# Kernel tuning notes

Hardware: AMD Instinct MI355X
Metric: run time of the kernel (lower is better)

## Reference

```python
import jax, jax.numpy as jnp
import numpy as np

B, N, E, D, R, T, L = 4, 20000, 320000, 64, 64, 1000, 6
LN_EPS = 1e-5


def setup_inputs() -> dict:
    key = jax.random.key(0)
    ks = jax.random.split(key, 20)
    inp = {
        "edge_index": jax.random.randint(ks[0], (2, E), 0, N),
        "edge_type": jax.random.randint(ks[1], (E,), 0, R),
        "relation_representations": jax.random.normal(ks[2], (B, R, D), jnp.float32),
        "h_index": jax.random.randint(ks[3], (B,), 0, N),
        "r_index": jax.random.randint(ks[4], (B,), 0, R),
        "t_index": jax.random.randint(ks[5], (B, T), 0, N),
        "edge_weight": jnp.ones((E,), jnp.float32),
        # per-layer relation-projection MLP (Linear,ReLU,Linear)
        "rp_w1": jax.random.normal(ks[6], (L, D, D), jnp.float32) / np.sqrt(D),
        "rp_b1": jnp.zeros((L, D), jnp.float32),
        "rp_w2": jax.random.normal(ks[7], (L, D, D), jnp.float32) / np.sqrt(D),
        "rp_b2": jnp.zeros((L, D), jnp.float32),
        # per-layer update linear: concat([input, aggregated]) -> D
        "conv_w": jax.random.normal(ks[8], (L, 2 * D, D), jnp.float32) / np.sqrt(2 * D),
        "conv_b": jnp.zeros((L, D), jnp.float32),
        "ln_g": jnp.ones((L, D), jnp.float32),
        "ln_b": jnp.zeros((L, D), jnp.float32),
        # final MLP (num_mlp_layers=2): feature_dim = D (last hidden) + D (query) = 2D
        "mlp_w1": jax.random.normal(ks[9], (2 * D, 2 * D), jnp.float32) / np.sqrt(2 * D),
        "mlp_b1": jnp.zeros((2 * D,), jnp.float32),
        "mlp_w2": jax.random.normal(ks[10], (2 * D, 1), jnp.float32) / np.sqrt(2 * D),
        "mlp_b2": jnp.zeros((1,), jnp.float32),
    }
    return inp


def reference(edge_index, edge_type, relation_representations, h_index, r_index,
              t_index, edge_weight, rp_w1, rp_b1, rp_w2, rp_b2, conv_w, conv_b,
              ln_g, ln_b, mlp_w1, mlp_b1, mlp_w2, mlp_b2):
    # --- boundary: scatter query embedding onto source node per query ---
    query = relation_representations[jnp.arange(B), r_index]              # [B, D]
    boundary = jnp.zeros((B, N, D), jnp.float32).at[jnp.arange(B), h_index].add(query)
    src, dst = edge_index[0], edge_index[1]

    def layer(x, params):
        w1, b1, w2, b2, cw, cb, g, b = params
        # project_relations MLP on query relation representations
        rel = jax.nn.relu(jnp.einsum('brd,de->bre', relation_representations, w1) + b1)
        rel = jnp.einsum('brd,de->bre', rel, w2) + b2                     # [B, R, D]
        # distmult message: h[src] * rel[edge_type], weighted
        msg = x[:, src, :] * rel[:, edge_type, :] * edge_weight[None, :, None]  # [B, E, D]
        agg = jax.ops.segment_sum(msg.transpose(1, 0, 2), dst,
                                  num_segments=N).transpose(1, 0, 2)
        agg = agg + boundary                                              # boundary self-loop
        h = jnp.concatenate([x, agg], axis=-1) @ cw + cb                  # [B, N, D]
        mu = h.mean(-1, keepdims=True)
        var = h.var(-1, keepdims=True)
        h = (h - mu) * jax.lax.rsqrt(var + LN_EPS) * g + b                # layer norm
        h = jax.nn.relu(h)
        return h + x, None                                                # short_cut

    x, _ = jax.lax.scan(layer, boundary,
                        (rp_w1, rp_b1, rp_w2, rp_b2, conv_w, conv_b, ln_g, ln_b))
    node_query = jnp.broadcast_to(query[:, None, :], (B, N, D))
    output = jnp.concatenate([x, node_query], axis=-1)                    # [B, N, 2D]
    feat = jnp.take_along_axis(output, t_index[:, :, None], axis=1)       # [B, T, 2D]
    h = jax.nn.relu(feat @ mlp_w1 + mlp_b1)
    score = (h @ mlp_w2 + mlp_b2).squeeze(-1)                             # [B, T]
    return score
```

## Files before the change

### kernel.cpp

```cpp
#include <hip/hip_runtime.h>
#include <hip/hip_fp16.h>

#define NB 4
#define NN 20000
#define NE 320000
#define ND 64
#define NR 64
#define NT 1000
#define NL 6
#define LN_EPS 1e-5f
#define CAP 64

typedef _Float16 half8 __attribute__((ext_vector_type(8)));
typedef _Float16 half4v __attribute__((ext_vector_type(4)));
typedef float floatx4 __attribute__((ext_vector_type(4)));


__global__ void __launch_bounds__(256)
prep1(int* __restrict__ cnt,
      const float* __restrict__ cw, _Float16* __restrict__ cwt,
      const float* __restrict__ relrep, const int* __restrict__ r_index,
      float* __restrict__ query,
      const float* __restrict__ rp_w1, const float* __restrict__ rp_b1,
      const float* __restrict__ rp_w2, const float* __restrict__ rp_b2,
      __half* __restrict__ rel16) {
    int blk = blockIdx.x, tid = threadIdx.x;
    if (blk < 79) {
        int i = blk * 256 + tid;
        if (i < NN) cnt[i] = 0;
    } else if (blk < 271) {
        int i = (blk - 79) * 256 + tid;
        int l = i >> 13, rem = i & 8191, k = rem >> 6, n = rem & 63;
        cwt[l * 8192 + n * 128 + k] = (_Float16)cw[i];
    } else if (blk == 271) {
        int b = tid >> 6, d = tid & 63;
        query[tid] = relrep[(b * NR + r_index[b]) * ND + d];
    } else {
        int u = blk - 272;
        int l = u >> 6, r = u & 63;
        int b = tid >> 6, j = tid & 63;
        const float* w1 = rp_w1 + l * ND * ND;
        const float* w2 = rp_w2 + l * ND * ND;
        float xin = relrep[(b * NR + r) * ND + j];
        float acc = rp_b1[l * ND + j];
        #pragma unroll 8
        for (int k = 0; k < ND; ++k) acc += __shfl(xin, k) * w1[k * ND + j];
        float hmid = fmaxf(acc, 0.f);
        float outv = rp_b2[l * ND + j];
        #pragma unroll 8
        for (int k = 0; k < ND; ++k) outv += __shfl(hmid, k) * w2[k * ND + j];
        rel16[l * (NR * NB * ND) + (r * NB + b) * ND + j] = __float2half(outv);
    }
}

__global__ void __launch_bounds__(256)
prep2(const int* __restrict__ ei, const int* __restrict__ et,
      const float* __restrict__ ew, int* __restrict__ cnt,
      int4* __restrict__ epack) {
    int e = blockIdx.x * 256 + threadIdx.x;
    int d = ei[NE + e];
    int p = atomicAdd(&cnt[d], 1);
    if (p < CAP)
        epack[d * CAP + p] = make_int4(ei[e], et[e], __float_as_int(ew[e]), 0);
}

__device__ __forceinline__ float2 h2f(unsigned u) {
    __half2 h = *(__half2*)&u;
    return __half22float2(h);
}
__device__ __forceinline__ __half2 u2h2(unsigned u) { return *(__half2*)&u; }

__device__ __forceinline__ void conv_ln_epilogue(
        _Float16* A16, float* sD, int wv, int lane, int n,
        const _Float16* __restrict__ cwt, const float* __restrict__ cb,
        const float* __restrict__ g, const float* __restrict__ bb,
        __half* __restrict__ xo16) {
    __syncthreads();
    {
        int m = lane & 15, quad = lane >> 4;
        int ncol = wv * 16 + m;
        floatx4 acc = {0.f, 0.f, 0.f, 0.f};
        #pragma unroll
        for (int k0 = 0; k0 < 128; k0 += 32) {
            half8 a = *(const half8*)&A16[m * 136 + k0 + quad * 8];
            half8 bfr = *(const half8*)&cwt[ncol * 128 + k0 + quad * 8];
            acc = __builtin_amdgcn_mfma_f32_16x16x32_f16(a, bfr, acc, 0, 0, 0);
        }
        #pragma unroll
        for (int rg = 0; rg < 4; ++rg)
            sD[(quad * 4 + rg) * 65 + ncol] = acc[rg];
    }
    __syncthreads();
    float gl = g[lane], bl = bb[lane], cbl = cb[lane];
    #pragma unroll
    for (int b = 0; b < NB; ++b) {
        float acc = sD[(wv * 4 + b) * 65 + lane] + cbl;
        float s = acc, s2 = acc * acc;
        #pragma unroll
        for (int o = 32; o > 0; o >>= 1) { s += __shfl_xor(s, o); s2 += __shfl_xor(s2, o); }
        float mu  = s * (1.f / ND);
        float var = s2 * (1.f / ND) - mu * mu;
        float hn  = (acc - mu) * rsqrtf(var + LN_EPS) * gl + bl;
        float xvf = (float)A16[(wv * 4 + b) * 136 + lane];
        float v   = fmaxf(hn, 0.f) + xvf;
        xo16[(n * NB + b) * ND + lane] = __float2half(v);
    }
}

__global__ void __launch_bounds__(256)
fused_layer_first(const __half* __restrict__ rel16,
                  const int* __restrict__ cnt, const int4* __restrict__ epack,
                  const float* __restrict__ query, const int* __restrict__ h_index,
                  const _Float16* __restrict__ cwt, const float* __restrict__ cb,
                  const float* __restrict__ g, const float* __restrict__ bb,
                  __half* __restrict__ xo16) {
    __shared__ _Float16 A16[16 * 136];
    __shared__ float sD[16 * 65];
    int wv = threadIdx.x >> 6;
    int lane = threadIdx.x & 63;
    int n = blockIdx.x * 4 + wv;
    int cn = min(cnt[n], CAP);
    int bidx = lane >> 4, c4 = (lane & 15) << 2;
    int hb = h_index[bidx];

    const uint2* __restrict__ r2 = (const uint2*)rel16;
    float4 q4 = ((const float4*)query)[lane];
    half4v qh;
    qh.x = (_Float16)q4.x; qh.y = (_Float16)q4.y;
    qh.z = (_Float16)q4.z; qh.w = (_Float16)q4.w;
    float qx = (float)qh.x, qy = (float)qh.y, qz = (float)qh.z, qw = (float)qh.w;

    float4 agg4 = make_float4(0.f, 0.f, 0.f, 0.f);
    {
        int4 ed = make_int4(0, 0, 0, 0);
        if (lane < cn) ed = epack[n * CAP + lane];
        for (int j = 0; j < cn; ++j) {
            int s   = __shfl(ed.x, j);
            int t   = __shfl(ed.y, j);
            float w = __int_as_float(__shfl(ed.z, j));
            if (s == hb) {
                uint2 ra = r2[t * 64 + lane];
                float2 q0 = h2f(ra.x), q1 = h2f(ra.y);
                agg4.x = fmaf(qx * q0.x, w, agg4.x);
                agg4.y = fmaf(qy * q0.y, w, agg4.y);
                agg4.z = fmaf(qz * q1.x, w, agg4.z);
                agg4.w = fmaf(qw * q1.y, w, agg4.w);
            }
        }
    }
    if (n == hb) {
        agg4.x += q4.x; agg4.y += q4.y; agg4.z += q4.z; agg4.w += q4.w;
    }
    {
        int r = wv * 4 + bidx;
        half4v xh = {0, 0, 0, 0};
        if (n == hb) xh = qh;
        *(half4v*)&A16[r * 136 + c4] = xh;
        half4v ah;
        ah.x = (_Float16)agg4.x; ah.y = (_Float16)agg4.y;
        ah.z = (_Float16)agg4.z; ah.w = (_Float16)agg4.w;
        *(half4v*)&A16[r * 136 + 64 + c4] = ah;
    }
    conv_ln_epilogue(A16, sD, wv, lane, n, cwt, cb, g, bb, xo16);
}

#define ACCUM(xv, rv, wv_) do {                                   \
    __half2 p0 = __hmul2(u2h2((xv).x), u2h2((rv).x));             \
    __half2 p1 = __hmul2(u2h2((xv).y), u2h2((rv).y));             \
    __half2 p2 = __hmul2(u2h2((xv).z), u2h2((rv).z));             \
    __half2 p3 = __hmul2(u2h2((xv).w), u2h2((rv).w));             \
    acc[0] = fmaf(__low2float(p0),  (wv_), acc[0]);               \
    acc[1] = fmaf(__high2float(p0), (wv_), acc[1]);               \
    acc[2] = fmaf(__low2float(p1),  (wv_), acc[2]);               \
    acc[3] = fmaf(__high2float(p1), (wv_), acc[3]);               \
    acc[4] = fmaf(__low2float(p2),  (wv_), acc[4]);               \
    acc[5] = fmaf(__high2float(p2), (wv_), acc[5]);               \
    acc[6] = fmaf(__low2float(p3),  (wv_), acc[6]);               \
    acc[7] = fmaf(__high2float(p3), (wv_), acc[7]);               \
} while (0)

__global__ void __launch_bounds__(256, 4)
fused_layer(const __half* __restrict__ x16, const __half* __restrict__ rel16,
            const int* __restrict__ cnt, const int4* __restrict__ epack,
            const float* __restrict__ query, const int* __restrict__ h_index,
            const _Float16* __restrict__ cwt, const float* __restrict__ cb,
            const float* __restrict__ g, const float* __restrict__ bb,
            __half* __restrict__ xo16) {
    __shared__ _Float16 A16[16 * 136];
    __shared__ float sD[16 * 65];
    int wv = threadIdx.x >> 6;
    int lane = threadIdx.x & 63;
    int n = blockIdx.x * 4 + wv;
    int cn = min(cnt[n], CAP);
    int hf = lane >> 5, sub = lane & 31;

    const uint4* __restrict__ x4 = (const uint4*)x16;
    const uint4* __restrict__ r4 = (const uint4*)rel16;

    const uint2* __restrict__ x2 = (const uint2*)x16;
    uint2 xraw = x2[(n * NB + (lane >> 4)) * 16 + (lane & 15)];

    float acc[8] = {0.f, 0.f, 0.f, 0.f, 0.f, 0.f, 0.f, 0.f};
    {
        int4 ed = make_int4(0, 0, 0, 0);
        if (lane < cn) ed = epack[n * CAP + lane];
        int cmax = (cn + 3) & ~3;
        if (cmax) {
            int ja = hf, jb = 2 + hf;
            int sa = __shfl(ed.x, ja), ta = __shfl(ed.y, ja);
            int sb = __shfl(ed.x, jb), tb = __shfl(ed.y, jb);
            float wa = __int_as_float(__shfl(ed.z, ja));
            float wb = __int_as_float(__shfl(ed.z, jb));
            uint4 xa = x4[sa * 32 + sub], ra = r4[ta * 32 + sub];
            uint4 xb = x4[sb * 32 + sub], rb = r4[tb * 32 + sub];
            for (int j = 4; j < cmax; j += 4) {
                int jc = j + hf, jd = j + 2 + hf;
                int sc = __shfl(ed.x, jc), tc = __shfl(ed.y, jc);
                int sd = __shfl(ed.x, jd), td = __shfl(ed.y, jd);
                float wc = __int_as_float(__shfl(ed.z, jc));
                float wd = __int_as_float(__shfl(ed.z, jd));
                uint4 xc = x4[sc * 32 + sub], rc = r4[tc * 32 + sub];
                uint4 xd = x4[sd * 32 + sub], rd = r4[td * 32 + sub];
                ACCUM(xa, ra, wa);
                ACCUM(xb, rb, wb);
                xa = xc; ra = rc; wa = wc;
                xb = xd; rb = rd; wb = wd;
            }
            ACCUM(xa, ra, wa);
            ACCUM(xb, rb, wb);
        }
    }
    #pragma unroll
    for (int k = 0; k < 8; ++k) acc[k] += __shfl_xor(acc[k], 32);
    int bq = sub >> 3, ch = (sub & 7) << 3;
    if (hf == 0) {
        if (n == h_index[bq]) {
            const float* qp = query + bq * 64 + ch;
            #pragma unroll
            for (int k = 0; k < 8; ++k) acc[k] += qp[k];
        }
        int r = wv * 4 + bq;
        half8 ah;
        #pragma unroll
        for (int k = 0; k < 8; ++k) ah[k] = (_Float16)acc[k];
        *(half8*)&A16[r * 136 + 64 + ch] = ah;
    }
    {
        int bidx = lane >> 4, c4 = (lane & 15) << 2;
        int r = wv * 4 + bidx;
        *(uint2*)&A16[r * 136 + c4] = xraw;
    }
    conv_ln_epilogue(A16, sD, wv, lane, n, cwt, cb, g, bb, xo16);
}

__global__ void final_score(const __half* __restrict__ x16, const float* __restrict__ query,
                            const int* __restrict__ t_index,
                            const float* __restrict__ w1, const float* __restrict__ b1,
                            const float* __restrict__ w2, const float* __restrict__ b2,
                            float* __restrict__ out) {
    int gid = blockIdx.x * 4 + (threadIdx.x >> 6);
    int lane = threadIdx.x & 63;
    int b = gid / NT;
    int ti = t_index[gid];
    float xv = __half2float(x16[(ti * NB + b) * ND + lane]);
    float qv = query[b * ND + lane];
    float a0 = b1[lane], a1 = b1[lane + 64];
    #pragma unroll 8
    for (int k = 0; k < ND; ++k) {
        float f = __shfl(xv, k);
        a0 += f * w1[k * 128 + lane];
        a1 += f * w1[k * 128 + lane + 64];
    }
    #pragma unroll 8
    for (int k = 0; k < ND; ++k) {
        float f = __shfl(qv, k);
        a0 += f * w1[(ND + k) * 128 + lane];
        a1 += f * w1[(ND + k) * 128 + lane + 64];
    }
    a0 = fmaxf(a0, 0.f);
    a1 = fmaxf(a1, 0.f);
    float p = a0 * w2[lane] + a1 * w2[lane + 64];
    #pragma unroll
    for (int o = 32; o > 0; o >>= 1) p += __shfl_xor(p, o);
    if (lane == 0) out[gid] = p + b2[0];
}

extern "C" void kernel_launch(void* const* d_in, const int* in_sizes, int n_in,
                              void* d_out, int out_size, void* d_ws, size_t ws_size,
                              hipStream_t stream) {
    const int*   edge_index  = (const int*)d_in[0];
    const int*   edge_type   = (const int*)d_in[1];
    const float* relrep      = (const float*)d_in[2];
    const int*   h_index     = (const int*)d_in[3];
    const int*   r_index     = (const int*)d_in[4];
    const int*   t_index     = (const int*)d_in[5];
    const float* edge_weight = (const float*)d_in[6];
    const float* rp_w1  = (const float*)d_in[7];
    const float* rp_b1  = (const float*)d_in[8];
    const float* rp_w2  = (const float*)d_in[9];
    const float* rp_b2  = (const float*)d_in[10];
    const float* conv_w = (const float*)d_in[11];
    const float* conv_b = (const float*)d_in[12];
    const float* ln_g   = (const float*)d_in[13];
    const float* ln_b   = (const float*)d_in[14];
    const float* mlp_w1 = (const float*)d_in[15];
    const float* mlp_b1 = (const float*)d_in[16];
    const float* mlp_w2 = (const float*)d_in[17];
    const float* mlp_b2 = (const float*)d_in[18];
    float* out = (float*)d_out;

    const int BND = NB * NN * ND;
    const int RELSZ = NR * NB * ND;
    float*    ws     = (float*)d_ws;
    float*    query  = ws;
    __half*   rel16  = (__half*)(query + 256);
    __half*   x16a   = rel16 + NL * RELSZ;
    __half*   x16b   = x16a + BND;
    _Float16* cwt16  = (_Float16*)(x16b + BND);
    int4*     epack  = (int4*)(cwt16 + NL * 8192);
    int*      cnt    = (int*)(epack + NN * CAP);

    prep1<<<656, 256, 0, stream>>>(cnt, conv_w, cwt16, relrep, r_index, query,
                                   rp_w1, rp_b1, rp_w2, rp_b2, rel16);
    prep2<<<NE / 256, 256, 0, stream>>>(edge_index, edge_type, edge_weight,
                                        cnt, epack);

    __half* mc = x16a; __half* mn = x16b;
    fused_layer_first<<<NN / 4, 256, 0, stream>>>(rel16, cnt, epack,
                                                  query, h_index,
                                                  cwt16, conv_b, ln_g, ln_b, mc);
    for (int l = 1; l < NL; ++l) {
        fused_layer<<<NN / 4, 256, 0, stream>>>(mc, rel16 + l * RELSZ, cnt, epack,
                                                query, h_index,
                                                cwt16 + l * 8192, conv_b + l * ND,
                                                ln_g + l * ND, ln_b + l * ND, mn);
        __half* th = mc; mc = mn; mn = th;
    }
    final_score<<<NB * NT / 4, 256, 0, stream>>>(mc, query, t_index,
                                                 mlp_w1, mlp_b1, mlp_w2, mlp_b2, out);
}
```

Before: 329.9 us.

## Sort nodes by in-degree so each block processes similar-degree nodes

```diff
diff --git a/kernel.cpp b/kernel.cpp
--- a/kernel.cpp
+++ b/kernel.cpp
@@ -20,7 +20,7 @@
 prep1(int* __restrict__ cnt,
       const float* __restrict__ cw, _Float16* __restrict__ cwt,
       const float* __restrict__ relrep, const int* __restrict__ r_index,
-      float* __restrict__ query,
+      float* __restrict__ query, int* __restrict__ hist,
       const float* __restrict__ rp_w1, const float* __restrict__ rp_b1,
       const float* __restrict__ rp_w2, const float* __restrict__ rp_b2,
       __half* __restrict__ rel16) {
@@ -35,6 +35,7 @@
     } else if (blk == 271) {
         int b = tid >> 6, d = tid & 63;
         query[tid] = relrep[(b * NR + r_index[b]) * ND + d];
+        if (tid < 96) hist[tid] = 0;
     } else {
         int u = blk - 272;
         int l = u >> 6, r = u & 63;
@@ -64,6 +65,29 @@
         epack[d * CAP + p] = make_int4(ei[e], et[e], __float_as_int(ew[e]), 0);
 }
 
+__global__ void __launch_bounds__(256)
+prep3a(const int* __restrict__ cnt, int* __restrict__ hist) {
+    int n = blockIdx.x * 256 + threadIdx.x;
+    if (n < NN) atomicAdd(&hist[min(cnt[n], CAP)], 1);
+}
+
+__global__ void prep3b(const int* __restrict__ hist, int* __restrict__ off) {
+    if (threadIdx.x == 0) {
+        int acc = 0;
+        for (int c = CAP; c >= 0; --c) { off[c] = acc; acc += hist[c]; }
+    }
+}
+
+__global__ void __launch_bounds__(256)
+prep3c(const int* __restrict__ cnt, int* __restrict__ off,
+       int* __restrict__ perm) {
+    int n = blockIdx.x * 256 + threadIdx.x;
+    if (n < NN) {
+        int p = atomicAdd(&off[min(cnt[n], CAP)], 1);
+        perm[p] = n;
+    }
+}
+
 __device__ __forceinline__ float2 h2f(unsigned u) {
     __half2 h = *(__half2*)&u;
     return __half22float2(h);
@@ -110,6 +134,7 @@
 __global__ void __launch_bounds__(256)
 fused_layer_first(const __half* __restrict__ rel16,
                   const int* __restrict__ cnt, const int4* __restrict__ epack,
+                  const int* __restrict__ perm,
                   const float* __restrict__ query, const int* __restrict__ h_index,
                   const _Float16* __restrict__ cwt, const float* __restrict__ cb,
                   const float* __restrict__ g, const float* __restrict__ bb,
@@ -118,7 +143,7 @@
     __shared__ float sD[16 * 65];
     int wv = threadIdx.x >> 6;
     int lane = threadIdx.x & 63;
-    int n = blockIdx.x * 4 + wv;
+    int n = perm[blockIdx.x * 4 + wv];
     int cn = min(cnt[n], CAP);
     int bidx = lane >> 4, c4 = (lane & 15) << 2;
     int hb = h_index[bidx];
@@ -182,6 +207,7 @@
 __global__ void __launch_bounds__(256, 4)
 fused_layer(const __half* __restrict__ x16, const __half* __restrict__ rel16,
             const int* __restrict__ cnt, const int4* __restrict__ epack,
+            const int* __restrict__ perm,
             const float* __restrict__ query, const int* __restrict__ h_index,
             const _Float16* __restrict__ cwt, const float* __restrict__ cb,
             const float* __restrict__ g, const float* __restrict__ bb,
@@ -190,7 +216,7 @@
     __shared__ float sD[16 * 65];
     int wv = threadIdx.x >> 6;
     int lane = threadIdx.x & 63;
-    int n = blockIdx.x * 4 + wv;
+    int n = perm[blockIdx.x * 4 + wv];
     int cn = min(cnt[n], CAP);
     int hf = lane >> 5, sub = lane & 31;
 
@@ -319,19 +345,25 @@
     _Float16* cwt16  = (_Float16*)(x16b + BND);
     int4*     epack  = (int4*)(cwt16 + NL * 8192);
     int*      cnt    = (int*)(epack + NN * CAP);
+    int*      perm   = cnt + NN;
+    int*      hist   = perm + NN;
+    int*      off    = hist + 96;
 
     prep1<<<656, 256, 0, stream>>>(cnt, conv_w, cwt16, relrep, r_index, query,
-                                   rp_w1, rp_b1, rp_w2, rp_b2, rel16);
+                                   hist, rp_w1, rp_b1, rp_w2, rp_b2, rel16);
     prep2<<<NE / 256, 256, 0, stream>>>(edge_index, edge_type, edge_weight,
                                         cnt, epack);
+    prep3a<<<79, 256, 0, stream>>>(cnt, hist);
+    prep3b<<<1, 64, 0, stream>>>(hist, off);
+    prep3c<<<79, 256, 0, stream>>>(cnt, off, perm);
 
     __half* mc = x16a; __half* mn = x16b;
-    fused_layer_first<<<NN / 4, 256, 0, stream>>>(rel16, cnt, epack,
+    fused_layer_first<<<NN / 4, 256, 0, stream>>>(rel16, cnt, epack, perm,
                                                   query, h_index,
                                                   cwt16, conv_b, ln_g, ln_b, mc);
     for (int l = 1; l < NL; ++l) {
         fused_layer<<<NN / 4, 256, 0, stream>>>(mc, rel16 + l * RELSZ, cnt, epack,
-                                                query, h_index,
+                                                perm, query, h_index,
                                                 cwt16 + l * 8192, conv_b + l * ND,
                                                 ln_g + l * ND, ln_b + l * ND, mn);
         __half* th = mc; mc = mn; mn = th;
```

Measured after the change: 438.8 us. 33.0% more time.

## Gather one edge per wave with uint2 loads and scalar readlane broadcasts

Applied to the files above, without the earlier changes.

```diff
diff --git a/kernel.cpp b/kernel.cpp
--- a/kernel.cpp
+++ b/kernel.cpp
@@ -119,7 +119,7 @@
     int wv = threadIdx.x >> 6;
     int lane = threadIdx.x & 63;
     int n = blockIdx.x * 4 + wv;
-    int cn = min(cnt[n], CAP);
+    int cn = __builtin_amdgcn_readfirstlane(min(cnt[n], CAP));
     int bidx = lane >> 4, c4 = (lane & 15) << 2;
     int hb = h_index[bidx];
 
@@ -135,9 +135,9 @@
         int4 ed = make_int4(0, 0, 0, 0);
         if (lane < cn) ed = epack[n * CAP + lane];
         for (int j = 0; j < cn; ++j) {
-            int s   = __shfl(ed.x, j);
-            int t   = __shfl(ed.y, j);
-            float w = __int_as_float(__shfl(ed.z, j));
+            int s   = __builtin_amdgcn_readlane(ed.x, j);
+            int t   = __builtin_amdgcn_readlane(ed.y, j);
+            float w = __int_as_float(__builtin_amdgcn_readlane(ed.z, j));
             if (s == hb) {
                 uint2 ra = r2[t * 64 + lane];
                 float2 q0 = h2f(ra.x), q1 = h2f(ra.y);
@@ -164,22 +164,7 @@
     conv_ln_epilogue(A16, sD, wv, lane, n, cwt, cb, g, bb, xo16);
 }
 
-#define ACCUM(xv, rv, wv_) do {                                   \
-    __half2 p0 = __hmul2(u2h2((xv).x), u2h2((rv).x));             \
-    __half2 p1 = __hmul2(u2h2((xv).y), u2h2((rv).y));             \
-    __half2 p2 = __hmul2(u2h2((xv).z), u2h2((rv).z));             \
-    __half2 p3 = __hmul2(u2h2((xv).w), u2h2((rv).w));             \
-    acc[0] = fmaf(__low2float(p0),  (wv_), acc[0]);               \
-    acc[1] = fmaf(__high2float(p0), (wv_), acc[1]);               \
-    acc[2] = fmaf(__low2float(p1),  (wv_), acc[2]);               \
-    acc[3] = fmaf(__high2float(p1), (wv_), acc[3]);               \
-    acc[4] = fmaf(__low2float(p2),  (wv_), acc[4]);               \
-    acc[5] = fmaf(__high2float(p2), (wv_), acc[5]);               \
-    acc[6] = fmaf(__low2float(p3),  (wv_), acc[6]);               \
-    acc[7] = fmaf(__high2float(p3), (wv_), acc[7]);               \
-} while (0)
-
-__global__ void __launch_bounds__(256, 4)
+__global__ void __launch_bounds__(256)
 fused_layer(const __half* __restrict__ x16, const __half* __restrict__ rel16,
             const int* __restrict__ cnt, const int4* __restrict__ epack,
             const float* __restrict__ query, const int* __restrict__ h_index,
@@ -191,63 +176,43 @@
     int wv = threadIdx.x >> 6;
     int lane = threadIdx.x & 63;
     int n = blockIdx.x * 4 + wv;
-    int cn = min(cnt[n], CAP);
-    int hf = lane >> 5, sub = lane & 31;
-
-    const uint4* __restrict__ x4 = (const uint4*)x16;
-    const uint4* __restrict__ r4 = (const uint4*)rel16;
+    int cn = __builtin_amdgcn_readfirstlane(min(cnt[n], CAP));
+    int bidx = lane >> 4, c4 = (lane & 15) << 2;
+    int hb = h_index[bidx];
 
     const uint2* __restrict__ x2 = (const uint2*)x16;
-    uint2 xraw = x2[(n * NB + (lane >> 4)) * 16 + (lane & 15)];
-
-    float acc[8] = {0.f, 0.f, 0.f, 0.f, 0.f, 0.f, 0.f, 0.f};
+    const uint2* __restrict__ r2 = (const uint2*)rel16;
+
+    uint2 xraw = x2[n * 64 + lane];
+
+    float4 acc = make_float4(0.f, 0.f, 0.f, 0.f);
     {
         int4 ed = make_int4(0, 0, 0, 0);
         if (lane < cn) ed = epack[n * CAP + lane];
-        int cmax = (cn + 3) & ~3;
-        if (cmax) {
-            int ja = hf, jb = 2 + hf;
-            int sa = __shfl(ed.x, ja), ta = __shfl(ed.y, ja);
-            int sb = __shfl(ed.x, jb), tb = __shfl(ed.y, jb);
-            float wa = __int_as_float(__shfl(ed.z, ja));
-            float wb = __int_as_float(__shfl(ed.z, jb));
-            uint4 xa = x4[sa * 32 + sub], ra = r4[ta * 32 + sub];
-            uint4 xb = x4[sb * 32 + sub], rb = r4[tb * 32 + sub];
-            for (int j = 4; j < cmax; j += 4) {
-                int jc = j + hf, jd = j + 2 + hf;
-                int sc = __shfl(ed.x, jc), tc = __shfl(ed.y, jc);
-                int sd = __shfl(ed.x, jd), td = __shfl(ed.y, jd);
-                float wc = __int_as_float(__shfl(ed.z, jc));
-                float wd = __int_as_float(__shfl(ed.z, jd));
-                uint4 xc = x4[sc * 32 + sub], rc = r4[tc * 32 + sub];
-                uint4 xd = x4[sd * 32 + sub], rd = r4[td * 32 + sub];
-                ACCUM(xa, ra, wa);
-                ACCUM(xb, rb, wb);
-                xa = xc; ra = rc; wa = wc;
-                xb = xd; rb = rd; wb = wd;
-            }
-            ACCUM(xa, ra, wa);
-            ACCUM(xb, rb, wb);
+        for (int j = 0; j < cn; ++j) {
+            int s   = __builtin_amdgcn_readlane(ed.x, j);
+            int t   = __builtin_amdgcn_readlane(ed.y, j);
+            float w = __int_as_float(__builtin_amdgcn_readlane(ed.z, j));
+            uint2 xa = x2[s * 64 + lane];
+            uint2 ra = r2[t * 64 + lane];
+            __half2 p0 = __hmul2(u2h2(xa.x), u2h2(ra.x));
+            __half2 p1 = __hmul2(u2h2(xa.y), u2h2(ra.y));
+            acc.x = fmaf(__low2float(p0),  w, acc.x);
+            acc.y = fmaf(__high2float(p0), w, acc.y);
+            acc.z = fmaf(__low2float(p1),  w, acc.z);
+            acc.w = fmaf(__high2float(p1), w, acc.w);
         }
     }
-    #pragma unroll
-    for (int k = 0; k < 8; ++k) acc[k] += __shfl_xor(acc[k], 32);
-    int bq = sub >> 3, ch = (sub & 7) << 3;
-    if (hf == 0) {
-        if (n == h_index[bq]) {
-            const float* qp = query + bq * 64 + ch;
-            #pragma unroll
-            for (int k = 0; k < 8; ++k) acc[k] += qp[k];
-        }
-        int r = wv * 4 + bq;
-        half8 ah;
-        #pragma unroll
-        for (int k = 0; k < 8; ++k) ah[k] = (_Float16)acc[k];
-        *(half8*)&A16[r * 136 + 64 + ch] = ah;
-    }
-    {
-        int bidx = lane >> 4, c4 = (lane & 15) << 2;
+    if (n == hb) {
+        const float4 q4 = ((const float4*)query)[lane];
+        acc.x += q4.x; acc.y += q4.y; acc.z += q4.z; acc.w += q4.w;
+    }
+    {
         int r = wv * 4 + bidx;
+        half4v ah;
+        ah.x = (_Float16)acc.x; ah.y = (_Float16)acc.y;
+        ah.z = (_Float16)acc.z; ah.w = (_Float16)acc.w;
+        *(half4v*)&A16[r * 136 + 64 + c4] = ah;
         *(uint2*)&A16[r * 136 + c4] = xraw;
     }
     conv_ln_epilogue(A16, sD, wv, lane, n, cwt, cb, g, bb, xo16);
```

After: 358.2 us. 8.6% more time.
